# Performance work log

Hardware: AMD Instinct MI355X
Metric: run time of the kernel (lower is better)

Reference implementation:

```python
import jax, jax.numpy as jnp
import numpy as np

STEPLIM = 20   # module steplim; loop runs while iter <= steplim -> steplim+1 iterations
TOL = 1e-4     # early-stopping tolerance on change in mean NN error


def _nn1(pc1, pc2):
    """1-NN of each point in pc1 [B,N,3] within pc2 [B,M,3] under L2 norm.
    Uses the GEMM form ||a||^2 + ||b||^2 - 2 a.b instead of materializing the
    [B,N,M,3] broadcasted difference tensor. Returns (min_dist [B,N], idx [B,N])."""
    d2 = (jnp.sum(pc1 * pc1, axis=-1)[..., :, None]
          + jnp.sum(pc2 * pc2, axis=-1)[..., None, :]
          - 2.0 * jnp.einsum('bnd,bmd->bnm', pc1, pc2))
    d2 = jnp.maximum(d2, 1e-12)                  # clamp FP cancellation negatives
    idx = jnp.argmin(d2, axis=-1)                # [B, N]
    dmin = jnp.sqrt(jnp.take_along_axis(d2, idx[..., None], axis=-1)[..., 0])
    return dmin, idx


def _kabsch(src, dst):
    """Rigid transform (R, t) minimizing ||R@src + t - dst|| via SVD (EPnP._points_transform)."""
    c1 = jnp.mean(src, axis=-2, keepdims=True)   # [B,1,3]
    c2 = jnp.mean(dst, axis=-2, keepdims=True)
    H = jnp.einsum('bni,bnj->bij', src - c1, dst - c2)          # [B,3,3]
    U, S, Vt = jnp.linalg.svd(H, full_matrices=False)
    det = jnp.linalg.det(jnp.einsum('bki,bjk->bij', Vt, U))     # det(V U^T)
    d = jnp.sign(det)
    D = jnp.stack([jnp.ones_like(d), jnp.ones_like(d), d], axis=-1)  # reflection fix
    R = jnp.einsum('bki,bk,bjk->bij', Vt, D, U)                 # V diag(1,1,d) U^T
    t = c2[..., 0, :] - jnp.einsum('bij,bj->bi', R, c1[..., 0, :])
    return R, t


def _icp(p1, p2):
    B = p1.shape[0]

    def step(carry, _):
        pc, err, done = carry
        dmin, idx = _nn1(pc, p2)
        # errnew = sum(sum(values)/len(values)): mean over batch of per-point sums
        errnew = jnp.sum(dmin) / B
        # source quirk: uses the LAST batch element's indices for all batches
        matched = p2[:, idx[-1], :]                              # [B,N,3]
        R, t = _kabsch(pc, matched)
        pc_new = jnp.einsum('bij,bnj->bni', R, pc) + t[:, None, :]
        # torch loop updates temppc BEFORE the break check, then freezes
        pc_out = jnp.where(done, pc, pc_new)
        err_out = jnp.where(done, err, errnew)
        done_out = done | (jnp.abs(err - errnew) < TOL)
        return (pc_out, err_out, done_out), None

    init = (p1, jnp.asarray(0.0, p1.dtype), jnp.asarray(False))
    (pc, _, _), _ = jax.lax.scan(step, init, None, length=STEPLIM + 1)
    R, t = _kabsch(p1, pc)
    return jnp.concatenate([R, t[..., None]], axis=-1)           # [B,3,4] = [R | t]


def setup_inputs() -> dict:
    key = jax.random.key(0)
    k1, k2 = jax.random.split(key)
    p1 = jax.random.normal(k1, (1, 8192, 3), dtype=jnp.float32)
    p2 = jax.random.normal(k2, (1, 8192, 3), dtype=jnp.float32)
    return {"p1": p1, "p2": p2}


def reference(p1, p2):
    return _icp(p1, p2)
```

## Files before the change

kernel.cpp:

```cpp
#include <hip/hip_runtime.h>
#include <math.h>

#define N_PTS 8192
#define ICP_STEPS 21
#define ICP_TOL 1e-4

#define NBLK 256
#define BSIZE 1024
#define QPW 8

struct IcpSt {
  double Rc[9];
  double tc[3];
  double err;
  int done;
};

__global__ __launch_bounds__(256) void icp_prep(const float* __restrict__ p2,
                                                float4* __restrict__ p2aug,
                                                IcpSt* __restrict__ st0) {
  int t = blockIdx.x * 256 + threadIdx.x;
  float x = p2[3*t], y = p2[3*t+1], z = p2[3*t+2];
  p2aug[t] = make_float4(x, y, z, fmaf(x, x, fmaf(y, y, z*z)));
  if (t == 0) {
    #pragma unroll
    for (int i = 0; i < 9; ++i) st0->Rc[i] = (i % 4 == 0) ? 1.0 : 0.0;
    st0->tc[0] = st0->tc[1] = st0->tc[2] = 0.0;
    st0->err = 0.0; st0->done = 0;
  }
}

__device__ __forceinline__ void kabsch_solve(const double* s, double* R, double* T) {
  const double n = (double)N_PTS;
  const double c1x = s[1]/n, c1y = s[2]/n, c1z = s[3]/n;
  const double c2x = s[4]/n, c2y = s[5]/n, c2z = s[6]/n;
  const double h00 = s[7]  - n*c1x*c2x, h01 = s[8]  - n*c1x*c2y, h02 = s[9]  - n*c1x*c2z;
  const double h10 = s[10] - n*c1y*c2x, h11 = s[11] - n*c1y*c2y, h12 = s[12] - n*c1y*c2z;
  const double h20 = s[13] - n*c1z*c2x, h21 = s[14] - n*c1z*c2y, h22 = s[15] - n*c1z*c2z;

  double a00 = h00*h00 + h10*h10 + h20*h20;
  double a01 = h00*h01 + h10*h11 + h20*h21;
  double a02 = h00*h02 + h10*h12 + h20*h22;
  double a11 = h01*h01 + h11*h11 + h21*h21;
  double a12 = h01*h02 + h11*h12 + h21*h22;
  double a22 = h02*h02 + h12*h12 + h22*h22;

  double v00=1.0, v01=0.0, v02=0.0;
  double v10=0.0, v11=1.0, v12=0.0;
  double v20=0.0, v21=0.0, v22=1.0;

#define ROT3(app, aqq, apq, arp, arq, vpa, vqa, vpb, vqb, vpc, vqc)              \
  {                                                                              \
    double apq_ = apq;                                                           \
    if (fabs(apq_) > 1e-300) {                                                   \
      double tau = (aqq - app) / (2.0 * apq_);                                   \
      double tt  = (tau >= 0.0 ? 1.0 : -1.0) / (fabs(tau) + sqrt(1.0 + tau*tau));\
      double c_  = 1.0 / sqrt(1.0 + tt*tt), sn = tt * c_;                        \
      app -= tt * apq_;  aqq += tt * apq_;  apq = 0.0;                           \
      double t1 = arp, t2 = arq;                                                 \
      arp = c_*t1 - sn*t2;  arq = sn*t1 + c_*t2;                                 \
      t1 = vpa; t2 = vqa; vpa = c_*t1 - sn*t2; vqa = sn*t1 + c_*t2;              \
      t1 = vpb; t2 = vqb; vpb = c_*t1 - sn*t2; vqb = sn*t1 + c_*t2;              \
      t1 = vpc; t2 = vqc; vpc = c_*t1 - sn*t2; vqc = sn*t1 + c_*t2;              \
    }                                                                            \
  }

  #pragma unroll
  for (int sweep = 0; sweep < 6; ++sweep) {
    ROT3(a00, a11, a01, a02, a12, v00, v01, v10, v11, v20, v21);
    ROT3(a00, a22, a02, a01, a12, v00, v02, v10, v12, v20, v22);
    ROT3(a11, a22, a12, a01, a02, v01, v02, v11, v12, v21, v22);
  }
#undef ROT3

  double l0 = a00, l1 = a11, l2 = a22;
  double e0x=v00, e0y=v10, e0z=v20;
  double e1x=v01, e1y=v11, e1z=v21;
  double e2x=v02, e2y=v12, e2z=v22;
#define CSWAP(la, lb, xa, ya, za, xb, yb, zb)                                    \
  if (lb > la) { double t_;                                                      \
    t_ = la; la = lb; lb = t_;  t_ = xa; xa = xb; xb = t_;                       \
    t_ = ya; ya = yb; yb = t_;  t_ = za; za = zb; zb = t_; }
  CSWAP(l0, l1, e0x, e0y, e0z, e1x, e1y, e1z);
  CSWAP(l0, l2, e0x, e0y, e0z, e2x, e2y, e2z);
  CSWAP(l1, l2, e1x, e1y, e1z, e2x, e2y, e2z);
#undef CSWAP

  double detV = e0x*(e1y*e2z - e1z*e2y) - e0y*(e1x*e2z - e1z*e2x)
              + e0z*(e1x*e2y - e1y*e2x);
  const double dsg = (detV >= 0.0) ? 1.0 : -1.0;

  double u0x = h00*e0x + h01*e0y + h02*e0z;
  double u0y = h10*e0x + h11*e0y + h12*e0z;
  double u0z = h20*e0x + h21*e0y + h22*e0z;
  double n0 = sqrt(u0x*u0x + u0y*u0y + u0z*u0z);
  if (!(n0 > 1e-150)) {
    R[0]=1.0; R[1]=0.0; R[2]=0.0; R[3]=0.0; R[4]=1.0; R[5]=0.0;
    R[6]=0.0; R[7]=0.0; R[8]=1.0;
    T[0]=c2x-c1x; T[1]=c2y-c1y; T[2]=c2z-c1z;
    return;
  }
  u0x /= n0; u0y /= n0; u0z /= n0;
  double u1x = h00*e1x + h01*e1y + h02*e1z;
  double u1y = h10*e1x + h11*e1y + h12*e1z;
  double u1z = h20*e1x + h21*e1y + h22*e1z;
  const double d10 = u1x*u0x + u1y*u0y + u1z*u0z;
  u1x -= d10*u0x; u1y -= d10*u0y; u1z -= d10*u0z;
  double n1 = sqrt(u1x*u1x + u1y*u1y + u1z*u1z);
  if (!(n1 > 1e-150)) {
    R[0]=1.0; R[1]=0.0; R[2]=0.0; R[3]=0.0; R[4]=1.0; R[5]=0.0;
    R[6]=0.0; R[7]=0.0; R[8]=1.0;
    T[0]=c2x-c1x; T[1]=c2y-c1y; T[2]=c2z-c1z;
    return;
  }
  u1x /= n1; u1y /= n1; u1z /= n1;
  const double u2x = u0y*u1z - u0z*u1y;
  const double u2y = u0z*u1x - u0x*u1z;
  const double u2z = u0x*u1y - u0y*u1x;

  R[0] = e0x*u0x + e1x*u1x + dsg*e2x*u2x;
  R[1] = e0x*u0y + e1x*u1y + dsg*e2x*u2y;
  R[2] = e0x*u0z + e1x*u1z + dsg*e2x*u2z;
  R[3] = e0y*u0x + e1y*u1x + dsg*e2y*u2x;
  R[4] = e0y*u0y + e1y*u1y + dsg*e2y*u2y;
  R[5] = e0y*u0z + e1y*u1z + dsg*e2y*u2z;
  R[6] = e0z*u0x + e1z*u1x + dsg*e2z*u2x;
  R[7] = e0z*u0y + e1z*u1y + dsg*e2z*u2y;
  R[8] = e0z*u0z + e1z*u1z + dsg*e2z*u2z;
  T[0] = c2x - (R[0]*c1x + R[1]*c1y + R[2]*c1z);
  T[1] = c2y - (R[3]*c1x + R[4]*c1y + R[5]*c1z);
  T[2] = c2z - (R[6]*c1x + R[7]*c1y + R[8]*c1z);
}

__device__ __forceinline__ void solve_compose(const double* s, const IcpSt* stIn,
                                              double* Rn, double* tn,
                                              double* errnew, int* dn) {
  double R[9], T[3];
  kabsch_solve(s, R, T);
  double Rc[9], tc[3];
  #pragma unroll
  for (int i = 0; i < 9; ++i) Rc[i] = stIn->Rc[i];
  #pragma unroll
  for (int i = 0; i < 3; ++i) tc[i] = stIn->tc[i];
  #pragma unroll
  for (int i = 0; i < 3; ++i) {
    #pragma unroll
    for (int j = 0; j < 3; ++j)
      Rn[3*i+j] = R[3*i+0]*Rc[0+j] + R[3*i+1]*Rc[3+j] + R[3*i+2]*Rc[6+j];
    tn[i] = R[3*i+0]*tc[0] + R[3*i+1]*tc[1] + R[3*i+2]*tc[2] + T[i];
  }
  *errnew = s[0];
  *dn = (fabs(stIn->err - *errnew) < ICP_TOL) ? 1 : 0;
}

__global__ __launch_bounds__(BSIZE) void icp_iter(const float* __restrict__ p1,
                                                  const float4* __restrict__ p2aug,
                                                  const IcpSt* __restrict__ stIn,
                                                  IcpSt* __restrict__ stOut,
                                                  const double* __restrict__ partIn,
                                                  double* __restrict__ partOut,
                                                  const int k) {
  __shared__ float4 cand[N_PTS];
  __shared__ double redbuf[64];
  __shared__ double RT[12];
  __shared__ int sdone;
  __shared__ unsigned long long pkbuf[32][4];
  __shared__ float4 qlds[32];
  __shared__ double pairbuf[32][17];

  const int tid  = threadIdx.x;
  const int lane = tid & 63;
  const int w    = tid >> 6;
  const int g    = w >> 2;
  const int s    = w & 3;

  if (stIn->done) {
    if (blockIdx.x == 0 && tid == 0) {
      #pragma unroll
      for (int i = 0; i < 9; ++i) stOut->Rc[i] = stIn->Rc[i];
      #pragma unroll
      for (int i = 0; i < 3; ++i) stOut->tc[i] = stIn->tc[i];
      stOut->err = stIn->err; stOut->done = 1;
    }
    return;
  }

  #pragma unroll
  for (int k2 = 0; k2 < 8; ++k2) {
    const int i = (k2 << 10) + tid;
    cand[i] = p2aug[i];
  }

  double R0, R1, R2, R3, R4, R5, R6, R7, R8, T0, T1, T2;
  if (k > 0) {
    double vv[16];
    if (tid < 256) {
      const double* row = partIn + (tid << 4);
      #pragma unroll
      for (int c = 0; c < 16; ++c) vv[c] = row[c];
    } else {
      #pragma unroll
      for (int c = 0; c < 16; ++c) vv[c] = 0.0;
    }
    if (w < 4) {
      #pragma unroll
      for (int q = 0; q < 16; ++q) {
        double x = vv[q];
        for (int o = 32; o > 0; o >>= 1) x += __shfl_down(x, o, 64);
        if (lane == 0) redbuf[w*16 + q] = x;
      }
    }
    __syncthreads();
    if (tid == 0) {
      double sm[16];
      #pragma unroll
      for (int i = 0; i < 16; ++i)
        sm[i] = redbuf[i] + redbuf[16+i] + redbuf[32+i] + redbuf[48+i];
      double Rn[9], tn[3], errnew; int dn;
      solve_compose(sm, stIn, Rn, tn, &errnew, &dn);
      #pragma unroll
      for (int i = 0; i < 9; ++i) stOut->Rc[i] = Rn[i];
      #pragma unroll
      for (int i = 0; i < 3; ++i) stOut->tc[i] = tn[i];
      stOut->err = errnew; stOut->done = dn;
      #pragma unroll
      for (int i = 0; i < 9; ++i) RT[i] = Rn[i];
      RT[9] = tn[0]; RT[10] = tn[1]; RT[11] = tn[2];
      sdone = dn;
    }
    __syncthreads();
    if (sdone) return;
    R0 = RT[0]; R1 = RT[1]; R2 = RT[2];
    R3 = RT[3]; R4 = RT[4]; R5 = RT[5];
    R6 = RT[6]; R7 = RT[7]; R8 = RT[8];
    T0 = RT[9]; T1 = RT[10]; T2 = RT[11];
  } else {
    R0 = stIn->Rc[0]; R1 = stIn->Rc[1]; R2 = stIn->Rc[2];
    R3 = stIn->Rc[3]; R4 = stIn->Rc[4]; R5 = stIn->Rc[5];
    R6 = stIn->Rc[6]; R7 = stIn->Rc[7]; R8 = stIn->Rc[8];
    T0 = stIn->tc[0]; T1 = stIn->tc[1]; T2 = stIn->tc[2];
  }

  const int qbase = (blockIdx.x << 5) + (g << 3);
  float axv[QPW], ayv[QPW], azv[QPW], best[QPW];
  int bidx[QPW];
  float qxr[QPW], qyr[QPW], qzr[QPW];
  #pragma unroll
  for (int j = 0; j < QPW; ++j) {
    const int q = qbase + j;
    const double X = (double)p1[3*q], Y = (double)p1[3*q+1], Z = (double)p1[3*q+2];
    qxr[j] = (float)(R0*X + R1*Y + R2*Z + T0);
    qyr[j] = (float)(R3*X + R4*Y + R5*Z + T1);
    qzr[j] = (float)(R6*X + R7*Y + R8*Z + T2);
    axv[j] = -2.f*qxr[j]; ayv[j] = -2.f*qyr[j]; azv[j] = -2.f*qzr[j];
    best[j] = __builtin_inff(); bidx[j] = 0;
  }
  if (s == 0 && lane == 0) {
    #pragma unroll
    for (int j = 0; j < QPW; ++j)
      qlds[(g << 3) + j] = make_float4(qxr[j], qyr[j], qzr[j], 0.f);
  }
  __syncthreads();

  const int cb = s << 11;
  #pragma unroll 8
  for (int kk = 0; kk < 32; ++kk) {
    const int cidx = cb + (kk << 6) + lane;
    float4 c = cand[cidx];
    #pragma unroll
    for (int j = 0; j < QPW; ++j) {
      float d = fmaf(axv[j], c.x, fmaf(ayv[j], c.y, fmaf(azv[j], c.z, c.w)));
      if (d < best[j]) { best[j] = d; bidx[j] = cidx; }
    }
  }

  unsigned long long pk[QPW];
  #pragma unroll
  for (int j = 0; j < QPW; ++j) {
    unsigned u = __float_as_uint(best[j]);
    u ^= (unsigned)((int)u >> 31) | 0x80000000u;
    pk[j] = ((unsigned long long)u << 32) | (unsigned)bidx[j];
  }
  #pragma unroll
  for (int j = 0; j < QPW; ++j) {
    #pragma unroll
    for (int o = 1; o < 64; o <<= 1) {
      unsigned long long other = __shfl_xor(pk[j], o, 64);
      pk[j] = (other < pk[j]) ? other : pk[j];
    }
  }
  if (lane == 0) {
    #pragma unroll
    for (int j = 0; j < QPW; ++j)
      pkbuf[(g << 3) + j][s] = pk[j];
  }
  __syncthreads();

  if (tid < 32) {
    unsigned long long m = pkbuf[tid][0];
    unsigned long long m1 = pkbuf[tid][1]; m = (m1 < m) ? m1 : m;
    unsigned long long m2 = pkbuf[tid][2]; m = (m2 < m) ? m2 : m;
    unsigned long long m3 = pkbuf[tid][3]; m = (m3 < m) ? m3 : m;
    const unsigned idx = (unsigned)(m & 0xffffffffull);
    const float4 q4 = qlds[tid];
    const float4 b4 = cand[idx];
    const double ax = q4.x, ay = q4.y, az = q4.z;
    const double bx = b4.x, by = b4.y, bz = b4.z;
    const double d2 = (ax*ax + ay*ay + az*az) + (bx*bx + by*by + bz*bz)
                    - 2.0*(ax*bx + ay*by + az*bz);
    pairbuf[tid][0]  = sqrt(fmax(d2, 1e-12));
    pairbuf[tid][1]  = ax;    pairbuf[tid][2]  = ay;    pairbuf[tid][3]  = az;
    pairbuf[tid][4]  = bx;    pairbuf[tid][5]  = by;    pairbuf[tid][6]  = bz;
    pairbuf[tid][7]  = ax*bx; pairbuf[tid][8]  = ax*by; pairbuf[tid][9]  = ax*bz;
    pairbuf[tid][10] = ay*bx; pairbuf[tid][11] = ay*by; pairbuf[tid][12] = ay*bz;
    pairbuf[tid][13] = az*bx; pairbuf[tid][14] = az*by; pairbuf[tid][15] = az*bz;
  }
  __syncthreads();

  if (tid < 16) {
    double ssum = 0.0;
    #pragma unroll
    for (int i = 0; i < 32; ++i) ssum += pairbuf[i][tid];
    partOut[(blockIdx.x << 4) + tid] = ssum;
  }
}

__global__ __launch_bounds__(256) void icp_final(const IcpSt* __restrict__ stIn,
                                                 const double* __restrict__ partIn,
                                                 float* __restrict__ out) {
  __shared__ double lds[64];
  __shared__ double tot[16];
  const int lane = threadIdx.x & 63;
  const int w    = threadIdx.x >> 6;

  if (stIn->done) {
    if (threadIdx.x == 0) {
      #pragma unroll
      for (int i = 0; i < 3; ++i) {
        out[4*i + 0] = (float)stIn->Rc[3*i + 0];
        out[4*i + 1] = (float)stIn->Rc[3*i + 1];
        out[4*i + 2] = (float)stIn->Rc[3*i + 2];
        out[4*i + 3] = (float)stIn->tc[i];
      }
    }
    return;
  }

  double v[16];
  const double* row = partIn + (threadIdx.x << 4);
  #pragma unroll
  for (int c = 0; c < 16; ++c) v[c] = row[c];
  #pragma unroll
  for (int q = 0; q < 16; ++q) {
    double x = v[q];
    for (int o = 32; o > 0; o >>= 1) x += __shfl_down(x, o, 64);
    if (lane == 0) lds[w*16 + q] = x;
  }
  __syncthreads();
  if (threadIdx.x < 16)
    tot[threadIdx.x] = lds[threadIdx.x] + lds[16 + threadIdx.x]
                     + lds[32 + threadIdx.x] + lds[48 + threadIdx.x];
  __syncthreads();

  if (threadIdx.x == 0) {
    double sm[16];
    #pragma unroll
    for (int i = 0; i < 16; ++i) sm[i] = tot[i];
    double Rn[9], tn[3], errnew; int dn;
    solve_compose(sm, stIn, Rn, tn, &errnew, &dn);
    #pragma unroll
    for (int i = 0; i < 3; ++i) {
      out[4*i + 0] = (float)Rn[3*i + 0];
      out[4*i + 1] = (float)Rn[3*i + 1];
      out[4*i + 2] = (float)Rn[3*i + 2];
      out[4*i + 3] = (float)tn[i];
    }
  }
}

extern "C" void kernel_launch(void* const* d_in, const int* in_sizes, int n_in,
                              void* d_out, int out_size, void* d_ws, size_t ws_size,
                              hipStream_t stream) {
  const float* p1 = (const float*)d_in[0];
  const float* p2 = (const float*)d_in[1];
  float* out = (float*)d_out;

  char* ws = (char*)d_ws;
  float4* p2aug = (float4*)ws;
  IcpSt* st0    = (IcpSt*)(ws + 128*1024);
  IcpSt* st1    = (IcpSt*)(ws + 128*1024 + 256);
  double* part0 = (double*)(ws + 128*1024 + 1024);
  double* part1 = (double*)(ws + 128*1024 + 1024 + 32*1024);

  IcpSt* st[2]    = { st0, st1 };
  double* part[2] = { part0, part1 };

  icp_prep<<<N_PTS/256, 256, 0, stream>>>(p2, p2aug, st0);
  for (int k = 0; k < ICP_STEPS; ++k) {
    const IcpSt* stIn   = (k == 0) ? st0 : st[(k-1) & 1];
    IcpSt* stOut        = st[k & 1];
    const double* pIn   = part[(k+1) & 1];
    double* pOut        = part[k & 1];
    if (k == 0) stOut = st1;
    icp_iter<<<NBLK, BSIZE, 0, stream>>>(p1, p2aug, stIn, stOut, pIn, pOut, k);
  }
  icp_final<<<1, 256, 0, stream>>>(st[0], part[0], out);
}
```

Before: 546.7 us.

## Shrink blocks to 256 threads and stream candidates through LDS in chunks

Each NN iteration block drops from 1024 to 256 threads. Every wave now scans all 8192 candidates for its own 8 queries, so the cross-wave min merge goes away. Candidates are staged through a 2048-entry LDS tile with register prefetch of the next chunk, which cuts LDS use from 128KB and allows more blocks per CU. The costs are four times as much scan work per wave, extra barriers per chunk, and fewer waves per block to hide latency.

```diff
diff --git a/kernel.cpp b/kernel.cpp
--- a/kernel.cpp
+++ b/kernel.cpp
@@ -5,9 +5,11 @@
 #define ICP_STEPS 21
 #define ICP_TOL 1e-4
 
-#define NBLK 256
-#define BSIZE 1024
-#define QPW 8
+#define NNB 256
+#define QPWv 8
+#define QPB 32
+#define CH 2048
+#define NCH 4
 
 struct IcpSt {
   double Rc[9];
@@ -153,26 +155,24 @@
   *dn = (fabs(stIn->err - *errnew) < ICP_TOL) ? 1 : 0;
 }
 
-__global__ __launch_bounds__(BSIZE) void icp_iter(const float* __restrict__ p1,
-                                                  const float4* __restrict__ p2aug,
-                                                  const IcpSt* __restrict__ stIn,
-                                                  IcpSt* __restrict__ stOut,
-                                                  const double* __restrict__ partIn,
-                                                  double* __restrict__ partOut,
-                                                  const int k) {
-  __shared__ float4 cand[N_PTS];
+__global__ __launch_bounds__(256) void icp_iter(const float* __restrict__ p1,
+                                                const float4* __restrict__ p2aug,
+                                                const IcpSt* __restrict__ stIn,
+                                                IcpSt* __restrict__ stOut,
+                                                const double* __restrict__ partIn,
+                                                double* __restrict__ partOut,
+                                                const int k) {
+  __shared__ float4 cand[CH];
   __shared__ double redbuf[64];
   __shared__ double RT[12];
   __shared__ int sdone;
-  __shared__ unsigned long long pkbuf[32][4];
-  __shared__ float4 qlds[32];
-  __shared__ double pairbuf[32][17];
+  __shared__ unsigned long long pkbuf[4][9];
+  __shared__ float4 qlds[QPB];
+  __shared__ double pairbuf[QPB][17];
 
   const int tid  = threadIdx.x;
   const int lane = tid & 63;
   const int w    = tid >> 6;
-  const int g    = w >> 2;
-  const int s    = w & 3;
 
   if (stIn->done) {
     if (blockIdx.x == 0 && tid == 0) {
@@ -185,30 +185,23 @@
     return;
   }
 
-  #pragma unroll
-  for (int k2 = 0; k2 < 8; ++k2) {
-    const int i = (k2 << 10) + tid;
-    cand[i] = p2aug[i];
-  }
+  float4 pf[8];
+  #pragma unroll
+  for (int kk = 0; kk < 8; ++kk) pf[kk] = p2aug[(kk << 8) + tid];
 
   double R0, R1, R2, R3, R4, R5, R6, R7, R8, T0, T1, T2;
   if (k > 0) {
     double vv[16];
-    if (tid < 256) {
+    {
       const double* row = partIn + (tid << 4);
       #pragma unroll
       for (int c = 0; c < 16; ++c) vv[c] = row[c];
-    } else {
-      #pragma unroll
-      for (int c = 0; c < 16; ++c) vv[c] = 0.0;
-    }
-    if (w < 4) {
-      #pragma unroll
-      for (int q = 0; q < 16; ++q) {
-        double x = vv[q];
-        for (int o = 32; o > 0; o >>= 1) x += __shfl_down(x, o, 64);
-        if (lane == 0) redbuf[w*16 + q] = x;
-      }
+    }
+    #pragma unroll
+    for (int q = 0; q < 16; ++q) {
+      double x = vv[q];
+      for (int o = 32; o > 0; o >>= 1) x += __shfl_down(x, o, 64);
+      if (lane == 0) redbuf[w*16 + q] = x;
     }
     __syncthreads();
     if (tid == 0) {
@@ -241,48 +234,53 @@
     T0 = stIn->tc[0]; T1 = stIn->tc[1]; T2 = stIn->tc[2];
   }
 
-  const int qbase = (blockIdx.x << 5) + (g << 3);
-  float axv[QPW], ayv[QPW], azv[QPW], best[QPW];
-  int bidx[QPW];
-  float qxr[QPW], qyr[QPW], qzr[QPW];
-  #pragma unroll
-  for (int j = 0; j < QPW; ++j) {
-    const int q = qbase + j;
+  const int qb = (blockIdx.x << 5) + (w << 3);
+  float axv[QPWv], ayv[QPWv], azv[QPWv], best[QPWv];
+  int bidx[QPWv];
+  #pragma unroll
+  for (int j = 0; j < QPWv; ++j) {
+    const int q = qb + j;
     const double X = (double)p1[3*q], Y = (double)p1[3*q+1], Z = (double)p1[3*q+2];
-    qxr[j] = (float)(R0*X + R1*Y + R2*Z + T0);
-    qyr[j] = (float)(R3*X + R4*Y + R5*Z + T1);
-    qzr[j] = (float)(R6*X + R7*Y + R8*Z + T2);
-    axv[j] = -2.f*qxr[j]; ayv[j] = -2.f*qyr[j]; azv[j] = -2.f*qzr[j];
+    const float qx = (float)(R0*X + R1*Y + R2*Z + T0);
+    const float qy = (float)(R3*X + R4*Y + R5*Z + T1);
+    const float qz = (float)(R6*X + R7*Y + R8*Z + T2);
+    axv[j] = -2.f*qx; ayv[j] = -2.f*qy; azv[j] = -2.f*qz;
     best[j] = __builtin_inff(); bidx[j] = 0;
-  }
-  if (s == 0 && lane == 0) {
-    #pragma unroll
-    for (int j = 0; j < QPW; ++j)
-      qlds[(g << 3) + j] = make_float4(qxr[j], qyr[j], qzr[j], 0.f);
-  }
-  __syncthreads();
-
-  const int cb = s << 11;
-  #pragma unroll 8
-  for (int kk = 0; kk < 32; ++kk) {
-    const int cidx = cb + (kk << 6) + lane;
-    float4 c = cand[cidx];
-    #pragma unroll
-    for (int j = 0; j < QPW; ++j) {
-      float d = fmaf(axv[j], c.x, fmaf(ayv[j], c.y, fmaf(azv[j], c.z, c.w)));
-      if (d < best[j]) { best[j] = d; bidx[j] = cidx; }
-    }
-  }
-
-  unsigned long long pk[QPW];
-  #pragma unroll
-  for (int j = 0; j < QPW; ++j) {
+    if (lane == 0) qlds[(w << 3) + j] = make_float4(qx, qy, qz, 0.f);
+  }
+
+  for (int cb = 0; cb < NCH; ++cb) {
+    #pragma unroll
+    for (int kk = 0; kk < 8; ++kk) cand[(kk << 8) + tid] = pf[kk];
+    __syncthreads();
+    if (cb + 1 < NCH) {
+      #pragma unroll
+      for (int kk = 0; kk < 8; ++kk)
+        pf[kk] = p2aug[((cb + 1) << 11) + (kk << 8) + tid];
+    }
+    const int cbase = cb << 11;
+    #pragma unroll 4
+    for (int kk = 0; kk < 32; ++kk) {
+      const int cidx = cbase + (kk << 6) + lane;
+      float4 c = cand[(kk << 6) + lane];
+      #pragma unroll
+      for (int j = 0; j < QPWv; ++j) {
+        float d = fmaf(axv[j], c.x, fmaf(ayv[j], c.y, fmaf(azv[j], c.z, c.w)));
+        if (d < best[j]) { best[j] = d; bidx[j] = cidx; }
+      }
+    }
+    __syncthreads();
+  }
+
+  unsigned long long pk[QPWv];
+  #pragma unroll
+  for (int j = 0; j < QPWv; ++j) {
     unsigned u = __float_as_uint(best[j]);
     u ^= (unsigned)((int)u >> 31) | 0x80000000u;
     pk[j] = ((unsigned long long)u << 32) | (unsigned)bidx[j];
   }
   #pragma unroll
-  for (int j = 0; j < QPW; ++j) {
+  for (int j = 0; j < QPWv; ++j) {
     #pragma unroll
     for (int o = 1; o < 64; o <<= 1) {
       unsigned long long other = __shfl_xor(pk[j], o, 64);
@@ -291,19 +289,15 @@
   }
   if (lane == 0) {
     #pragma unroll
-    for (int j = 0; j < QPW; ++j)
-      pkbuf[(g << 3) + j][s] = pk[j];
+    for (int j = 0; j < QPWv; ++j) pkbuf[w][j] = pk[j];
   }
   __syncthreads();
 
-  if (tid < 32) {
-    unsigned long long m = pkbuf[tid][0];
-    unsigned long long m1 = pkbuf[tid][1]; m = (m1 < m) ? m1 : m;
-    unsigned long long m2 = pkbuf[tid][2]; m = (m2 < m) ? m2 : m;
-    unsigned long long m3 = pkbuf[tid][3]; m = (m3 < m) ? m3 : m;
+  if (tid < QPB) {
+    const unsigned long long m = pkbuf[tid >> 3][tid & 7];
     const unsigned idx = (unsigned)(m & 0xffffffffull);
     const float4 q4 = qlds[tid];
-    const float4 b4 = cand[idx];
+    const float4 b4 = p2aug[idx];
     const double ax = q4.x, ay = q4.y, az = q4.z;
     const double bx = b4.x, by = b4.y, bz = b4.z;
     const double d2 = (ax*ax + ay*ay + az*az) + (bx*bx + by*by + bz*bz)
@@ -318,18 +312,17 @@
   __syncthreads();
 
   if (tid < 16) {
-    double ssum = 0.0;
-    #pragma unroll
-    for (int i = 0; i < 32; ++i) ssum += pairbuf[i][tid];
-    partOut[(blockIdx.x << 4) + tid] = ssum;
+    double s = 0.0;
+    #pragma unroll
+    for (int i = 0; i < QPB; ++i) s += pairbuf[i][tid];
+    partOut[(blockIdx.x << 4) + tid] = s;
   }
 }
 
 __global__ __launch_bounds__(256) void icp_final(const IcpSt* __restrict__ stIn,
                                                  const double* __restrict__ partIn,
                                                  float* __restrict__ out) {
-  __shared__ double lds[64];
-  __shared__ double tot[16];
+  __shared__ double redbuf[64];
   const int lane = threadIdx.x & 63;
   const int w    = threadIdx.x >> 6;
 
@@ -346,26 +339,25 @@
     return;
   }
 
-  double v[16];
-  const double* row = partIn + (threadIdx.x << 4);
-  #pragma unroll
-  for (int c = 0; c < 16; ++c) v[c] = row[c];
+  double vv[16];
+  {
+    const double* row = partIn + (threadIdx.x << 4);
+    #pragma unroll
+    for (int c = 0; c < 16; ++c) vv[c] = row[c];
+  }
   #pragma unroll
   for (int q = 0; q < 16; ++q) {
-    double x = v[q];
+    double x = vv[q];
     for (int o = 32; o > 0; o >>= 1) x += __shfl_down(x, o, 64);
-    if (lane == 0) lds[w*16 + q] = x;
-  }
-  __syncthreads();
-  if (threadIdx.x < 16)
-    tot[threadIdx.x] = lds[threadIdx.x] + lds[16 + threadIdx.x]
-                     + lds[32 + threadIdx.x] + lds[48 + threadIdx.x];
+    if (lane == 0) redbuf[w*16 + q] = x;
+  }
   __syncthreads();
 
   if (threadIdx.x == 0) {
     double sm[16];
     #pragma unroll
-    for (int i = 0; i < 16; ++i) sm[i] = tot[i];
+    for (int i = 0; i < 16; ++i)
+      sm[i] = redbuf[i] + redbuf[16+i] + redbuf[32+i] + redbuf[48+i];
     double Rn[9], tn[3], errnew; int dn;
     solve_compose(sm, stIn, Rn, tn, &errnew, &dn);
     #pragma unroll
@@ -402,7 +394,7 @@
     const double* pIn   = part[(k+1) & 1];
     double* pOut        = part[k & 1];
     if (k == 0) stOut = st1;
-    icp_iter<<<NBLK, BSIZE, 0, stream>>>(p1, p2aug, stIn, stOut, pIn, pOut, k);
+    icp_iter<<<NNB, 256, 0, stream>>>(p1, p2aug, stIn, stOut, pIn, pOut, k);
   }
   icp_final<<<1, 256, 0, stream>>>(st[0], part[0], out);
 }
```

Measured after the change: 803.2 us. +46.9%, slower.
